# Optimization experiments

Hardware: AMD Instinct MI355X
Metric: run time of the kernel (lower is better)

Reference implementation:

```python
import jax, jax.numpy as jnp
import numpy as np

B = 4096   # batch
C = 1024   # per-node channels


def setup_inputs() -> dict:
    key = jax.random.key(0)
    k0, k1, k2, k3, k4 = jax.random.split(key, 5)
    x0 = jax.random.normal(k0, (B, C), dtype=jnp.float32)
    x1 = jax.random.normal(k1, (B, C), dtype=jnp.float32)
    # per-edge DNet weights: edge_in=concat (2 heads -> 2C) -> matmul W -> edge_out=split (2 tails of C)
    scale = 0.02
    W0 = jax.random.normal(k2, (2 * C, 2 * C), dtype=jnp.float32) * scale
    W1 = jax.random.normal(k3, (2 * C, 2 * C), dtype=jnp.float32) * scale
    W2 = jax.random.normal(k4, (2 * C, 2 * C), dtype=jnp.float32) * scale
    return {"x0": x0, "x1": x1, "W0": W0, "W1": W1, "W2": W2}


def _edge(head_a, head_b, W):
    # MHD_concat over sorted head nodes (dim=1), DNet matmul, MHD_split into tail node channels
    z = jnp.concatenate([head_a, head_b], axis=1) @ W  # [B, 2C]
    return z[:, :C], z[:, C:]  # two tail tensors [B, C]


def reference(x0, x1, W0, W1, W2):
    # DAG routing in topological order (MHD_topological_sort of the role matrix):
    # edge0: heads (n0, n1) -> tails (n2, n3)
    # edge1: heads (n2, n3) -> tails (n4, n5)
    # edge2: heads (n4, n5) -> tails (n6, n7)
    # node_tail_func = 'sum' (single contribution per tail here)
    n2, n3 = _edge(x0, x1, W0)
    n4, n5 = _edge(n2, n3, W1)
    n6, n7 = _edge(n4, n5, W2)
    # output: concat of terminal nodes (sorted order)
    return jnp.concatenate([n6, n7], axis=1)  # [B, 2C]
```

## Files before the change

kernel.cpp:

```cpp
#include <hip/hip_runtime.h>
#include <hip/hip_bf16.h>
#include <stdint.h>

typedef __bf16 bf16;
typedef __bf16 bf16x8 __attribute__((ext_vector_type(8)));
typedef float f32x4 __attribute__((ext_vector_type(4)));

#define GAS __attribute__((address_space(1)))
#define LAS __attribute__((address_space(3)))

static constexpr int M = 4096;
static constexpr int N = 2048;
static constexpr int K = 2048;

static constexpr int BM = 128, BN = 256, BK = 64;
static constexpr int NT = K / BK;
static constexpr int A_ELE = BM * BK;
static constexpr int B_ELE = BN * BK;
static constexpr int BUF_ELE = A_ELE + B_ELE;

static constexpr int WA_ELE = 64 * BK;
static constexpr int WB_ELE = 128 * BK;
static constexpr int WBUF_ELE = WA_ELE + WB_ELE;

__device__ __forceinline__ void gload_lds16(const bf16* gsrc, bf16* ldst) {
    __builtin_amdgcn_global_load_lds((const GAS void*)gsrc, (LAS void*)ldst, 16, 0, 0);
}

__global__ __launch_bounds__(256) void prep_kernel(const float* __restrict__ x0,
                                                   const float* __restrict__ x1,
                                                   const float* __restrict__ W0,
                                                   const float* __restrict__ W1,
                                                   const float* __restrict__ W2,
                                                   bf16* __restrict__ Xpk,
                                                   bf16* __restrict__ W0pk,
                                                   bf16* __restrict__ W1t,
                                                   bf16* __restrict__ W2t) {
    __shared__ bf16 tile[32][33];
    int bid = blockIdx.x;
    int tid = threadIdx.x;
    if (bid < 4096) {
        int idx = (bid * 256 + tid) * 8;
        int b = idx >> 11;
        int c = idx & 2047;
        const float* src = (c < 1024) ? (x0 + (size_t)b * 1024 + c)
                                      : (x1 + (size_t)b * 1024 + (c - 1024));
        float4 v0 = *reinterpret_cast<const float4*>(src);
        float4 v1 = *reinterpret_cast<const float4*>(src + 4);
        bf16x8 o;
        o[0] = (bf16)v0.x; o[1] = (bf16)v0.y; o[2] = (bf16)v0.z; o[3] = (bf16)v0.w;
        o[4] = (bf16)v1.x; o[5] = (bf16)v1.y; o[6] = (bf16)v1.z; o[7] = (bf16)v1.w;
        *reinterpret_cast<bf16x8*>(Xpk + idx) = o;
    } else if (bid < 6144) {
        int idx = ((bid - 4096) * 256 + tid) * 8;
        float4 v0 = *reinterpret_cast<const float4*>(W0 + idx);
        float4 v1 = *reinterpret_cast<const float4*>(W0 + idx + 4);
        bf16x8 o;
        o[0] = (bf16)v0.x; o[1] = (bf16)v0.y; o[2] = (bf16)v0.z; o[3] = (bf16)v0.w;
        o[4] = (bf16)v1.x; o[5] = (bf16)v1.y; o[6] = (bf16)v1.z; o[7] = (bf16)v1.w;
        *reinterpret_cast<bf16x8*>(W0pk + idx) = o;
    } else {
        int r = bid - 6144;
        int w = r >> 12;
        int t = r & 4095;
        const float* W  = (w == 0) ? W1  : W2;
        bf16*        Wt = (w == 0) ? W1t : W2t;
        int n0 = (t & 63) * 32;
        int k0 = (t >> 6) * 32;
        int tx = tid & 31;
        int ty = tid >> 5;
        #pragma unroll
        for (int i = 0; i < 4; i++) {
            int k = ty + i * 8;
            tile[k][tx] = (bf16)W[(size_t)(k0 + k) * N + n0 + tx];
        }
        __syncthreads();
        #pragma unroll
        for (int i = 0; i < 4; i++) {
            int n = ty + i * 8;
            Wt[(size_t)(n0 + n) * K + k0 + tx] = tile[tx][n];
        }
    }
}

__device__ __forceinline__ void read_frags(const bf16* __restrict__ ba, const bf16* __restrict__ bb,
                                           int aoff, int boff, int slot,
                                           bf16x8 af[4], bf16x8 bv[4]) {
    #pragma unroll
    for (int mi = 0; mi < 4; mi++)
        af[mi] = *reinterpret_cast<const bf16x8*>(ba + aoff + mi * 1024 + slot);
    #pragma unroll
    for (int ni = 0; ni < 4; ni++)
        bv[ni] = *reinterpret_cast<const bf16x8*>(bb + boff + ni * 1024 + slot);
}

__device__ __forceinline__ void do_mfma16(const bf16x8 af[4], const bf16x8 bv[4], f32x4 acc[4][4]) {
    __builtin_amdgcn_s_setprio(1);
    #pragma unroll
    for (int mi = 0; mi < 4; mi++)
        #pragma unroll
        for (int ni = 0; ni < 4; ni++)
            acc[mi][ni] = __builtin_amdgcn_mfma_f32_16x16x32_bf16(af[mi], bv[ni], acc[mi][ni], 0, 0, 0);
    __builtin_amdgcn_s_setprio(0);
}

__global__ __launch_bounds__(512, 2) void gemmx_kernel(const bf16* __restrict__ A,
                                                       const bf16* __restrict__ Bt,
                                                       float* __restrict__ Cout) {
    __shared__ bf16 lds[3 * BUF_ELE];

    int bid = blockIdx.x;
    int cpx = gridDim.x >> 3;
    int swz = (bid & 7) * cpx + (bid >> 3);
    int tm = swz >> 3;
    int tn = swz & 7;

    int tid  = threadIdx.x;
    int wave = tid >> 6;
    int lane = tid & 63;
    int wr = wave >> 2;
    int wc = wave & 3;
    int fr = lane & 15;
    int fb = lane >> 4;

    int srow = wave * 8 + (lane >> 3);
    int scol = ((lane & 7) ^ (lane >> 3)) * 8;
    const bf16* aS = A  + (size_t)(tm * BM + srow) * K + scol;
    const bf16* bS = Bt + (size_t)(tn * BN + srow) * K + scol;
    int sdst = wave * 512;

    int aoff  = (wr * 64 + fr) * 64;
    int boff  = (wc * 64 + fr) * 64;
    int slot0 = ((fb) ^ (fr & 7)) * 8;
    int slot1 = ((4 | fb) ^ (fr & 7)) * 8;

    f32x4 acc[4][4] = {};

    auto STAGE = [&](int bi, int t) {
        bf16* ba = (bf16*)lds + bi * BUF_ELE;
        bf16* bb = ba + A_ELE;
        const bf16* a = aS + t * BK;
        const bf16* b = bS + t * BK;
        gload_lds16(a,           ba + sdst);
        gload_lds16(a + 64 * K,  ba + sdst + 4096);
        gload_lds16(b,           bb + sdst);
        gload_lds16(b + 64 * K,  bb + sdst + 4096);
        gload_lds16(b + 128 * K, bb + sdst + 8192);
        gload_lds16(b + 192 * K, bb + sdst + 12288);
    };

    STAGE(0, 0);
    STAGE(1, 1);
    asm volatile("s_waitcnt vmcnt(6)" ::: "memory");
    __builtin_amdgcn_s_barrier();

    bf16x8 af0[4], bv0[4], af1[4], bv1[4];
    int cur = 0;
    for (int t = 0; t < NT - 2; ++t) {
        const bf16* ba = (const bf16*)lds + cur * BUF_ELE;
        const bf16* bb = ba + A_ELE;
        int sb = cur + 2; if (sb >= 3) sb -= 3;

        read_frags(ba, bb, aoff, boff, slot0, af0, bv0);
        read_frags(ba, bb, aoff, boff, slot1, af1, bv1);
        STAGE(sb, t + 2);
        asm volatile("s_waitcnt lgkmcnt(8)" ::: "memory");
        __builtin_amdgcn_sched_barrier(0);
        do_mfma16(af0, bv0, acc);
        asm volatile("s_waitcnt lgkmcnt(0)" ::: "memory");
        __builtin_amdgcn_sched_barrier(0);
        do_mfma16(af1, bv1, acc);
        asm volatile("s_waitcnt vmcnt(6)" ::: "memory");
        __builtin_amdgcn_s_barrier();
        cur = cur + 1; if (cur >= 3) cur -= 3;
    }
    {
        const bf16* ba = (const bf16*)lds + cur * BUF_ELE;
        const bf16* bb = ba + A_ELE;
        read_frags(ba, bb, aoff, boff, slot0, af0, bv0);
        read_frags(ba, bb, aoff, boff, slot1, af1, bv1);
        asm volatile("s_waitcnt lgkmcnt(8)" ::: "memory");
        __builtin_amdgcn_sched_barrier(0);
        do_mfma16(af0, bv0, acc);
        asm volatile("s_waitcnt lgkmcnt(0)" ::: "memory");
        __builtin_amdgcn_sched_barrier(0);
        do_mfma16(af1, bv1, acc);
        asm volatile("s_waitcnt vmcnt(0)" ::: "memory");
        __builtin_amdgcn_s_barrier();
        cur = cur + 1; if (cur >= 3) cur -= 3;
    }
    {
        const bf16* ba = (const bf16*)lds + cur * BUF_ELE;
        const bf16* bb = ba + A_ELE;
        read_frags(ba, bb, aoff, boff, slot0, af0, bv0);
        read_frags(ba, bb, aoff, boff, slot1, af1, bv1);
        asm volatile("s_waitcnt lgkmcnt(8)" ::: "memory");
        __builtin_amdgcn_sched_barrier(0);
        do_mfma16(af0, bv0, acc);
        asm volatile("s_waitcnt lgkmcnt(0)" ::: "memory");
        __builtin_amdgcn_sched_barrier(0);
        do_mfma16(af1, bv1, acc);
    }

    int row0 = tm * BM + wr * 64 + (lane >> 4) * 4;
    int col0 = tn * BN + wc * 64 + (lane & 15);
    #pragma unroll
    for (int mi = 0; mi < 4; mi++)
        #pragma unroll
        for (int r = 0; r < 4; r++) {
            size_t base = (size_t)(row0 + mi * 16 + r) * N + col0;
            #pragma unroll
            for (int ni = 0; ni < 4; ni++)
                Cout[base + ni * 16] = acc[mi][ni][r];
        }
}

__global__ __launch_bounds__(256, 2) void gemmw_kernel(const bf16* __restrict__ A,
                                                       const bf16* __restrict__ Bt,
                                                       bf16* __restrict__ C) {
    __shared__ bf16 lds[3 * WBUF_ELE];

    int bid = blockIdx.x;
    int cpx = gridDim.x >> 3;
    int swz = (bid & 7) * cpx + (bid >> 3);
    int tm = swz >> 4;
    int tn = swz & 15;

    int tid  = threadIdx.x;
    int wave = tid >> 6;
    int lane = tid & 63;
    int wr = wave >> 1;
    int wc = wave & 1;
    int fr = lane & 15;
    int fb = lane >> 4;

    int srow = tid >> 3;
    int scol = ((tid & 7) ^ (srow & 7)) * 8;
    const bf16* aS = A  + (size_t)(tm * 64  + srow) * K + scol;
    const bf16* bS = Bt + (size_t)(tn * 128 + srow) * K + scol;
    int sdst = wave * 512;

    int aoff  = (wr * 32 + fr) * 64;
    int boff  = (wc * 64 + fr) * 64;
    int slot0 = ((fb) ^ (fr & 7)) * 8;
    int slot1 = ((4 | fb) ^ (fr & 7)) * 8;

    f32x4 acc[2][4] = {};

    auto STAGE = [&](int bi, int t) {
        bf16* ba = (bf16*)lds + bi * WBUF_ELE;
        bf16* bb = ba + WA_ELE;
        const bf16* a = aS + t * BK;
        const bf16* b = bS + t * BK;
        gload_lds16(a,          ba + sdst);
        gload_lds16(a + 32 * K, ba + sdst + 2048);
        #pragma unroll
        for (int c = 0; c < 4; c++)
            gload_lds16(b + (size_t)c * 32 * K, bb + sdst + c * 2048);
    };

    auto READ = [&](const bf16* ba, const bf16* bb, int slot, bf16x8 af[2], bf16x8 bv[4]) {
        af[0] = *reinterpret_cast<const bf16x8*>(ba + aoff + slot);
        af[1] = *reinterpret_cast<const bf16x8*>(ba + aoff + 1024 + slot);
        #pragma unroll
        for (int ni = 0; ni < 4; ni++)
            bv[ni] = *reinterpret_cast<const bf16x8*>(bb + boff + ni * 1024 + slot);
    };

    auto MFMA8 = [&](const bf16x8 af[2], const bf16x8 bv[4]) {
        __builtin_amdgcn_s_setprio(1);
        #pragma unroll
        for (int mi = 0; mi < 2; mi++)
            #pragma unroll
            for (int ni = 0; ni < 4; ni++)
                acc[mi][ni] = __builtin_amdgcn_mfma_f32_16x16x32_bf16(af[mi], bv[ni], acc[mi][ni], 0, 0, 0);
        __builtin_amdgcn_s_setprio(0);
    };

    STAGE(0, 0);
    STAGE(1, 1);
    asm volatile("s_waitcnt vmcnt(6)" ::: "memory");
    __builtin_amdgcn_s_barrier();

    bf16x8 af0[2], bv0[4], af1[2], bv1[4];
    int cur = 0;
    for (int t = 0; t < NT - 2; ++t) {
        const bf16* ba = (const bf16*)lds + cur * WBUF_ELE;
        const bf16* bb = ba + WA_ELE;
        int sb = cur + 2; if (sb >= 3) sb -= 3;

        READ(ba, bb, slot0, af0, bv0);
        READ(ba, bb, slot1, af1, bv1);
        STAGE(sb, t + 2);
        asm volatile("s_waitcnt lgkmcnt(6)" ::: "memory");
        __builtin_amdgcn_sched_barrier(0);
        MFMA8(af0, bv0);
        asm volatile("s_waitcnt lgkmcnt(0)" ::: "memory");
        __builtin_amdgcn_sched_barrier(0);
        MFMA8(af1, bv1);
        asm volatile("s_waitcnt vmcnt(6)" ::: "memory");
        __builtin_amdgcn_s_barrier();
        cur = cur + 1; if (cur >= 3) cur -= 3;
    }
    {
        const bf16* ba = (const bf16*)lds + cur * WBUF_ELE;
        const bf16* bb = ba + WA_ELE;
        READ(ba, bb, slot0, af0, bv0);
        READ(ba, bb, slot1, af1, bv1);
        asm volatile("s_waitcnt lgkmcnt(6)" ::: "memory");
        __builtin_amdgcn_sched_barrier(0);
        MFMA8(af0, bv0);
        asm volatile("s_waitcnt lgkmcnt(0)" ::: "memory");
        __builtin_amdgcn_sched_barrier(0);
        MFMA8(af1, bv1);
        asm volatile("s_waitcnt vmcnt(0)" ::: "memory");
        __builtin_amdgcn_s_barrier();
        cur = cur + 1; if (cur >= 3) cur -= 3;
    }
    {
        const bf16* ba = (const bf16*)lds + cur * WBUF_ELE;
        const bf16* bb = ba + WA_ELE;
        READ(ba, bb, slot0, af0, bv0);
        READ(ba, bb, slot1, af1, bv1);
        asm volatile("s_waitcnt lgkmcnt(6)" ::: "memory");
        __builtin_amdgcn_sched_barrier(0);
        MFMA8(af0, bv0);
        asm volatile("s_waitcnt lgkmcnt(0)" ::: "memory");
        __builtin_amdgcn_sched_barrier(0);
        MFMA8(af1, bv1);
    }

    int row0 = tm * 64 + wr * 32 + (lane >> 4) * 4;
    int col0 = tn * 128 + wc * 64 + fr;
    #pragma unroll
    for (int mi = 0; mi < 2; mi++)
        #pragma unroll
        for (int r = 0; r < 4; r++) {
            size_t base = (size_t)(row0 + mi * 16 + r) * 2048 + col0;
            #pragma unroll
            for (int ni = 0; ni < 4; ni++)
                C[base + ni * 16] = (bf16)acc[mi][ni][r];
        }
}

extern "C" void kernel_launch(void* const* d_in, const int* in_sizes, int n_in,
                              void* d_out, int out_size, void* d_ws, size_t ws_size,
                              hipStream_t stream) {
    const float* x0 = (const float*)d_in[0];
    const float* x1 = (const float*)d_in[1];
    const float* W0 = (const float*)d_in[2];
    const float* W1 = (const float*)d_in[3];
    const float* W2 = (const float*)d_in[4];

    char* ws = (char*)d_ws;
    const size_t MB = 1024 * 1024;
    bf16* Xpk    = (bf16*)(ws + 0 * MB);
    bf16* W1t    = (bf16*)(ws + 16 * MB);
    bf16* W012t  = (bf16*)(ws + 16 * MB);
    bf16* W2t    = (bf16*)(ws + 24 * MB);
    bf16* W01    = (bf16*)(ws + 32 * MB);
    bf16* W0pk   = (bf16*)d_out;

    prep_kernel<<<4096 + 2048 + 2 * 4096, 256, 0, stream>>>(x0, x1, W0, W1, W2,
                                                            Xpk, W0pk, W1t, W2t);

    gemmw_kernel<<<(2048 / 64) * (2048 / 128), 256, 0, stream>>>(W0pk, W1t, W01);
    gemmw_kernel<<<(2048 / 64) * (2048 / 128), 256, 0, stream>>>(W2t, W01, W012t);
    gemmx_kernel<<<(M / BM) * (N / BN), 512, 0, stream>>>(Xpk, W012t, (float*)d_out);
}
```

Measured before the change: 101.1 us.

## Fold W2 transpose and x packing into the weight GEMM launches

Splits the monolithic prep kernel so that W2's transpose runs as extra blocks inside the first weight-product GEMM launch, and the x0/x1 bf16 packing runs as extra blocks inside the second. Weight-GEMM blocks can then overlap with independent memory-bound conversion work, filling idle CUs in the 512-block GEMM grids. The GEMM main loops are also manually unrolled by three with constant buffer indices, and the split lgkmcnt waits and sched barriers between the two MFMA halves are dropped. This leaves instruction ordering to the compiler and may change how LDS reads overlap with MFMAs.

After: 101.2 us. About the same (+0.0%).

```diff
diff --git a/kernel.cpp b/kernel.cpp
--- a/kernel.cpp
+++ b/kernel.cpp
@@ -22,86 +22,194 @@
 static constexpr int WA_ELE = 64 * BK;
 static constexpr int WB_ELE = 128 * BK;
 static constexpr int WBUF_ELE = WA_ELE + WB_ELE;
+static constexpr int WGRID = 512;
 
 __device__ __forceinline__ void gload_lds16(const bf16* gsrc, bf16* ldst) {
     __builtin_amdgcn_global_load_lds((const GAS void*)gsrc, (LAS void*)ldst, 16, 0, 0);
 }
 
-__global__ __launch_bounds__(256) void prep_kernel(const float* __restrict__ x0,
-                                                   const float* __restrict__ x1,
-                                                   const float* __restrict__ W0,
-                                                   const float* __restrict__ W1,
-                                                   const float* __restrict__ W2,
-                                                   bf16* __restrict__ Xpk,
-                                                   bf16* __restrict__ W0pk,
-                                                   bf16* __restrict__ W1t,
-                                                   bf16* __restrict__ W2t) {
+__device__ __forceinline__ void pack8(const float* __restrict__ src, bf16* __restrict__ dst) {
+    float4 v0 = *reinterpret_cast<const float4*>(src);
+    float4 v1 = *reinterpret_cast<const float4*>(src + 4);
+    bf16x8 o;
+    o[0] = (bf16)v0.x; o[1] = (bf16)v0.y; o[2] = (bf16)v0.z; o[3] = (bf16)v0.w;
+    o[4] = (bf16)v1.x; o[5] = (bf16)v1.y; o[6] = (bf16)v1.z; o[7] = (bf16)v1.w;
+    *reinterpret_cast<bf16x8*>(dst) = o;
+}
+
+__device__ __forceinline__ void transpose_tile(const float* __restrict__ W, bf16* __restrict__ Wt,
+                                               int t, int tid, bf16 (*tile)[33]) {
+    int n0 = (t & 63) * 32;
+    int k0 = (t >> 6) * 32;
+    int tx = tid & 31;
+    int ty = tid >> 5;
+    #pragma unroll
+    for (int i = 0; i < 4; i++) {
+        int k = ty + i * 8;
+        tile[k][tx] = (bf16)W[(size_t)(k0 + k) * N + n0 + tx];
+    }
+    __syncthreads();
+    #pragma unroll
+    for (int i = 0; i < 4; i++) {
+        int n = ty + i * 8;
+        Wt[(size_t)(n0 + n) * K + k0 + tx] = tile[tx][n];
+    }
+}
+
+__device__ __forceinline__ void gemmw_body(const bf16* __restrict__ A,
+                                           const bf16* __restrict__ Bt,
+                                           bf16* __restrict__ C,
+                                           int bid, bf16* lds) {
+    int swz = (bid & 7) * (WGRID >> 3) + (bid >> 3);
+    int tm = swz >> 4;
+    int tn = swz & 15;
+
+    int tid  = threadIdx.x;
+    int wave = tid >> 6;
+    int lane = tid & 63;
+    int wr = wave >> 1;
+    int wc = wave & 1;
+    int fr = lane & 15;
+    int fb = lane >> 4;
+
+    int srow = tid >> 3;
+    int scol = ((tid & 7) ^ (srow & 7)) * 8;
+    const bf16* aS = A  + (size_t)(tm * 64  + srow) * K + scol;
+    const bf16* bS = Bt + (size_t)(tn * 128 + srow) * K + scol;
+    int sdst = wave * 512;
+
+    int aoff  = (wr * 32 + fr) * 64;
+    int boff  = (wc * 64 + fr) * 64;
+    int slot0 = ((fb) ^ (fr & 7)) * 8;
+    int slot1 = ((4 | fb) ^ (fr & 7)) * 8;
+
+    f32x4 acc[2][4] = {};
+    bf16x8 af0[2], bv0[4], af1[2], bv1[4];
+
+    auto STAGE = [&](int bi, int t) {
+        bf16* ba = lds + bi * WBUF_ELE;
+        bf16* bb = ba + WA_ELE;
+        const bf16* a = aS + t * BK;
+        const bf16* b = bS + t * BK;
+        gload_lds16(a,          ba + sdst);
+        gload_lds16(a + 32 * K, ba + sdst + 2048);
+        #pragma unroll
+        for (int c = 0; c < 4; c++)
+            gload_lds16(b + (size_t)c * 32 * K, bb + sdst + c * 2048);
+    };
+    auto READ = [&](const bf16* ba, const bf16* bb, int slot, bf16x8 af[2], bf16x8 bv[4]) {
+        af[0] = *reinterpret_cast<const bf16x8*>(ba + aoff + slot);
+        af[1] = *reinterpret_cast<const bf16x8*>(ba + aoff + 1024 + slot);
+        #pragma unroll
+        for (int ni = 0; ni < 4; ni++)
+            bv[ni] = *reinterpret_cast<const bf16x8*>(bb + boff + ni * 1024 + slot);
+    };
+    auto MFMA8 = [&](const bf16x8 af[2], const bf16x8 bv[4]) {
+        #pragma unroll
+        for (int mi = 0; mi < 2; mi++)
+            #pragma unroll
+            for (int ni = 0; ni < 4; ni++)
+                acc[mi][ni] = __builtin_amdgcn_mfma_f32_16x16x32_bf16(af[mi], bv[ni], acc[mi][ni], 0, 0, 0);
+    };
+    auto TILE = [&](int t, int cb, int sb) {
+        const bf16* ba = lds + cb * WBUF_ELE;
+        const bf16* bb = ba + WA_ELE;
+        READ(ba, bb, slot0, af0, bv0);
+        READ(ba, bb, slot1, af1, bv1);
+        STAGE(sb, t + 2);
+        __builtin_amdgcn_s_setprio(1);
+        MFMA8(af0, bv0);
+        MFMA8(af1, bv1);
+        __builtin_amdgcn_s_setprio(0);
+        asm volatile("s_waitcnt lgkmcnt(0)" ::: "memory");
+        asm volatile("s_waitcnt vmcnt(6)" ::: "memory");
+        __builtin_amdgcn_s_barrier();
+    };
+
+    STAGE(0, 0);
+    STAGE(1, 1);
+    asm volatile("s_waitcnt vmcnt(6)" ::: "memory");
+    __builtin_amdgcn_s_barrier();
+
+    for (int i = 0; i < 10; ++i) {
+        TILE(3 * i,     0, 2);
+        TILE(3 * i + 1, 1, 0);
+        TILE(3 * i + 2, 2, 1);
+    }
+    {
+        const bf16* ba = lds;
+        const bf16* bb = ba + WA_ELE;
+        READ(ba, bb, slot0, af0, bv0);
+        READ(ba, bb, slot1, af1, bv1);
+        MFMA8(af0, bv0);
+        MFMA8(af1, bv1);
+        asm volatile("s_waitcnt lgkmcnt(0)" ::: "memory");
+        asm volatile("s_waitcnt vmcnt(0)" ::: "memory");
+        __builtin_amdgcn_s_barrier();
+    }
+    {
+        const bf16* ba = lds + WBUF_ELE;
+        const bf16* bb = ba + WA_ELE;
+        READ(ba, bb, slot0, af0, bv0);
+        READ(ba, bb, slot1, af1, bv1);
+        MFMA8(af0, bv0);
+        MFMA8(af1, bv1);
+    }
+
+    int row0 = tm * 64 + wr * 32 + (lane >> 4) * 4;
+    int col0 = tn * 128 + wc * 64 + fr;
+    #pragma unroll
+    for (int mi = 0; mi < 2; mi++)
+        #pragma unroll
+        for (int r = 0; r < 4; r++) {
+            size_t base = (size_t)(row0 + mi * 16 + r) * 2048 + col0;
+            #pragma unroll
+            for (int ni = 0; ni < 4; ni++)
+                C[base + ni * 16] = (bf16)acc[mi][ni][r];
+        }
+}
+
+__global__ __launch_bounds__(256) void k1_prep(const float* __restrict__ W0, bf16* __restrict__ W0pk,
+                                               const float* __restrict__ W1, bf16* __restrict__ W1t) {
     __shared__ bf16 tile[32][33];
     int bid = blockIdx.x;
     int tid = threadIdx.x;
-    if (bid < 4096) {
+    if (bid < 2048) {
         int idx = (bid * 256 + tid) * 8;
+        pack8(W0 + idx, W0pk + idx);
+    } else {
+        transpose_tile(W1, W1t, bid - 2048, tid, tile);
+    }
+}
+
+__global__ __launch_bounds__(256, 2) void g1_fused(const bf16* __restrict__ A, const bf16* __restrict__ Bt,
+                                                   bf16* __restrict__ C,
+                                                   const float* __restrict__ W2, bf16* __restrict__ W2t) {
+    __shared__ bf16 lds[3 * WBUF_ELE];
+    int bid = blockIdx.x;
+    if (bid < WGRID) {
+        gemmw_body(A, Bt, C, bid, lds);
+    } else {
+        transpose_tile(W2, W2t, bid - WGRID, threadIdx.x, (bf16(*)[33])lds);
+    }
+}
+
+__global__ __launch_bounds__(256, 2) void g2_fused(const bf16* __restrict__ A, const bf16* __restrict__ Bt,
+                                                   bf16* __restrict__ C,
+                                                   const float* __restrict__ x0, const float* __restrict__ x1,
+                                                   bf16* __restrict__ Xpk) {
+    __shared__ bf16 lds[3 * WBUF_ELE];
+    int bid = blockIdx.x;
+    if (bid < WGRID) {
+        gemmw_body(A, Bt, C, bid, lds);
+    } else {
+        int idx = ((bid - WGRID) * 256 + threadIdx.x) * 8;
         int b = idx >> 11;
         int c = idx & 2047;
         const float* src = (c < 1024) ? (x0 + (size_t)b * 1024 + c)
                                       : (x1 + (size_t)b * 1024 + (c - 1024));
-        float4 v0 = *reinterpret_cast<const float4*>(src);
-        float4 v1 = *reinterpret_cast<const float4*>(src + 4);
-        bf16x8 o;
-        o[0] = (bf16)v0.x; o[1] = (bf16)v0.y; o[2] = (bf16)v0.z; o[3] = (bf16)v0.w;
-        o[4] = (bf16)v1.x; o[5] = (bf16)v1.y; o[6] = (bf16)v1.z; o[7] = (bf16)v1.w;
-        *reinterpret_cast<bf16x8*>(Xpk + idx) = o;
-    } else if (bid < 6144) {
-        int idx = ((bid - 4096) * 256 + tid) * 8;
-        float4 v0 = *reinterpret_cast<const float4*>(W0 + idx);
-        float4 v1 = *reinterpret_cast<const float4*>(W0 + idx + 4);
-        bf16x8 o;
-        o[0] = (bf16)v0.x; o[1] = (bf16)v0.y; o[2] = (bf16)v0.z; o[3] = (bf16)v0.w;
-        o[4] = (bf16)v1.x; o[5] = (bf16)v1.y; o[6] = (bf16)v1.z; o[7] = (bf16)v1.w;
-        *reinterpret_cast<bf16x8*>(W0pk + idx) = o;
-    } else {
-        int r = bid - 6144;
-        int w = r >> 12;
-        int t = r & 4095;
-        const float* W  = (w == 0) ? W1  : W2;
-        bf16*        Wt = (w == 0) ? W1t : W2t;
-        int n0 = (t & 63) * 32;
-        int k0 = (t >> 6) * 32;
-        int tx = tid & 31;
-        int ty = tid >> 5;
-        #pragma unroll
-        for (int i = 0; i < 4; i++) {
-            int k = ty + i * 8;
-            tile[k][tx] = (bf16)W[(size_t)(k0 + k) * N + n0 + tx];
-        }
-        __syncthreads();
-        #pragma unroll
-        for (int i = 0; i < 4; i++) {
-            int n = ty + i * 8;
-            Wt[(size_t)(n0 + n) * K + k0 + tx] = tile[tx][n];
-        }
-    }
-}
-
-__device__ __forceinline__ void read_frags(const bf16* __restrict__ ba, const bf16* __restrict__ bb,
-                                           int aoff, int boff, int slot,
-                                           bf16x8 af[4], bf16x8 bv[4]) {
-    #pragma unroll
-    for (int mi = 0; mi < 4; mi++)
-        af[mi] = *reinterpret_cast<const bf16x8*>(ba + aoff + mi * 1024 + slot);
-    #pragma unroll
-    for (int ni = 0; ni < 4; ni++)
-        bv[ni] = *reinterpret_cast<const bf16x8*>(bb + boff + ni * 1024 + slot);
-}
-
-__device__ __forceinline__ void do_mfma16(const bf16x8 af[4], const bf16x8 bv[4], f32x4 acc[4][4]) {
-    __builtin_amdgcn_s_setprio(1);
-    #pragma unroll
-    for (int mi = 0; mi < 4; mi++)
-        #pragma unroll
-        for (int ni = 0; ni < 4; ni++)
-            acc[mi][ni] = __builtin_amdgcn_mfma_f32_16x16x32_bf16(af[mi], bv[ni], acc[mi][ni], 0, 0, 0);
-    __builtin_amdgcn_s_setprio(0);
+        pack8(src, Xpk + idx);
+    }
 }
 
 __global__ __launch_bounds__(512, 2) void gemmx_kernel(const bf16* __restrict__ A,
@@ -135,6 +243,7 @@
     int slot1 = ((4 | fb) ^ (fr & 7)) * 8;
 
     f32x4 acc[4][4] = {};
+    bf16x8 af0[4], bv0[4], af1[4], bv1[4];
 
     auto STAGE = [&](int bi, int t) {
         bf16* ba = (bf16*)lds + bi * BUF_ELE;
@@ -148,58 +257,64 @@
         gload_lds16(b + 128 * K, bb + sdst + 8192);
         gload_lds16(b + 192 * K, bb + sdst + 12288);
     };
+    auto READ = [&](const bf16* ba, const bf16* bb, int slot, bf16x8 af[4], bf16x8 bv[4]) {
+        #pragma unroll
+        for (int mi = 0; mi < 4; mi++)
+            af[mi] = *reinterpret_cast<const bf16x8*>(ba + aoff + mi * 1024 + slot);
+        #pragma unroll
+        for (int ni = 0; ni < 4; ni++)
+            bv[ni] = *reinterpret_cast<const bf16x8*>(bb + boff + ni * 1024 + slot);
+    };
+    auto MFMA16 = [&](const bf16x8 af[4], const bf16x8 bv[4]) {
+        #pragma unroll
+        for (int mi = 0; mi < 4; mi++)
+            #pragma unroll
+            for (int ni = 0; ni < 4; ni++)
+                acc[mi][ni] = __builtin_amdgcn_mfma_f32_16x16x32_bf16(af[mi], bv[ni], acc[mi][ni], 0, 0, 0);
+    };
+    auto TILE = [&](int t, int cb, int sb) {
+        const bf16* ba = (const bf16*)lds + cb * BUF_ELE;
+        const bf16* bb = ba + A_ELE;
+        READ(ba, bb, slot0, af0, bv0);
+        READ(ba, bb, slot1, af1, bv1);
+        STAGE(sb, t + 2);
+        __builtin_amdgcn_s_setprio(1);
+        MFMA16(af0, bv0);
+        MFMA16(af1, bv1);
+        __builtin_amdgcn_s_setprio(0);
+        asm volatile("s_waitcnt lgkmcnt(0)" ::: "memory");
+        asm volatile("s_waitcnt vmcnt(6)" ::: "memory");
+        __builtin_amdgcn_s_barrier();
+    };
 
     STAGE(0, 0);
     STAGE(1, 1);
     asm volatile("s_waitcnt vmcnt(6)" ::: "memory");
     __builtin_amdgcn_s_barrier();
 
-    bf16x8 af0[4], bv0[4], af1[4], bv1[4];
-    int cur = 0;
-    for (int t = 0; t < NT - 2; ++t) {
-        const bf16* ba = (const bf16*)lds + cur * BUF_ELE;
+    for (int i = 0; i < 10; ++i) {
+        TILE(3 * i,     0, 2);
+        TILE(3 * i + 1, 1, 0);
+        TILE(3 * i + 2, 2, 1);
+    }
+    {
+        const bf16* ba = (const bf16*)lds;
         const bf16* bb = ba + A_ELE;
-        int sb = cur + 2; if (sb >= 3) sb -= 3;
-
-        read_frags(ba, bb, aoff, boff, slot0, af0, bv0);
-        read_frags(ba, bb, aoff, boff, slot1, af1, bv1);
-        STAGE(sb, t + 2);
-        asm volatile("s_waitcnt lgkmcnt(8)" ::: "memory");
-        __builtin_amdgcn_sched_barrier(0);
-        do_mfma16(af0, bv0, acc);
+        READ(ba, bb, slot0, af0, bv0);
+        READ(ba, bb, slot1, af1, bv1);
+        MFMA16(af0, bv0);
+        MFMA16(af1, bv1);
         asm volatile("s_waitcnt lgkmcnt(0)" ::: "memory");
-        __builtin_amdgcn_sched_barrier(0);
-        do_mfma16(af1, bv1, acc);
-        asm volatile("s_waitcnt vmcnt(6)" ::: "memory");
-        __builtin_amdgcn_s_barrier();
-        cur = cur + 1; if (cur >= 3) cur -= 3;
-    }
-    {
-        const bf16* ba = (const bf16*)lds + cur * BUF_ELE;
-        const bf16* bb = ba + A_ELE;
-        read_frags(ba, bb, aoff, boff, slot0, af0, bv0);
-        read_frags(ba, bb, aoff, boff, slot1, af1, bv1);
-        asm volatile("s_waitcnt lgkmcnt(8)" ::: "memory");
-        __builtin_amdgcn_sched_barrier(0);
-        do_mfma16(af0, bv0, acc);
-        asm volatile("s_waitcnt lgkmcnt(0)" ::: "memory");
-        __builtin_amdgcn_sched_barrier(0);
-        do_mfma16(af1, bv1, acc);
         asm volatile("s_waitcnt vmcnt(0)" ::: "memory");
         __builtin_amdgcn_s_barrier();
-        cur = cur + 1; if (cur >= 3) cur -= 3;
     }
     {
-        const bf16* ba = (const bf16*)lds + cur * BUF_ELE;
+        const bf16* ba = (const bf16*)lds + BUF_ELE;
         const bf16* bb = ba + A_ELE;
-        read_frags(ba, bb, aoff, boff, slot0, af0, bv0);
-        read_frags(ba, bb, aoff, boff, slot1, af1, bv1);
-        asm volatile("s_waitcnt lgkmcnt(8)" ::: "memory");
-        __builtin_amdgcn_sched_barrier(0);
-        do_mfma16(af0, bv0, acc);
-        asm volatile("s_waitcnt lgkmcnt(0)" ::: "memory");
-        __builtin_amdgcn_sched_barrier(0);
-        do_mfma16(af1, bv1, acc);
+        READ(ba, bb, slot0, af0, bv0);
+        READ(ba, bb, slot1, af1, bv1);
+        MFMA16(af0, bv0);
+        MFMA16(af1, bv1);
     }
 
     int row0 = tm * BM + wr * 64 + (lane >> 4) * 4;
@@ -212,134 +327,6 @@
             #pragma unroll
             for (int ni = 0; ni < 4; ni++)
                 Cout[base + ni * 16] = acc[mi][ni][r];
-        }
-}
-
-__global__ __launch_bounds__(256, 2) void gemmw_kernel(const bf16* __restrict__ A,
-                                                       const bf16* __restrict__ Bt,
-                                                       bf16* __restrict__ C) {
-    __shared__ bf16 lds[3 * WBUF_ELE];
-
-    int bid = blockIdx.x;
-    int cpx = gridDim.x >> 3;
-    int swz = (bid & 7) * cpx + (bid >> 3);
-    int tm = swz >> 4;
-    int tn = swz & 15;
-
-    int tid  = threadIdx.x;
-    int wave = tid >> 6;
-    int lane = tid & 63;
-    int wr = wave >> 1;
-    int wc = wave & 1;
-    int fr = lane & 15;
-    int fb = lane >> 4;
-
-    int srow = tid >> 3;
-    int scol = ((tid & 7) ^ (srow & 7)) * 8;
-    const bf16* aS = A  + (size_t)(tm * 64  + srow) * K + scol;
-    const bf16* bS = Bt + (size_t)(tn * 128 + srow) * K + scol;
-    int sdst = wave * 512;
-
-    int aoff  = (wr * 32 + fr) * 64;
-    int boff  = (wc * 64 + fr) * 64;
-    int slot0 = ((fb) ^ (fr & 7)) * 8;
-    int slot1 = ((4 | fb) ^ (fr & 7)) * 8;
-
-    f32x4 acc[2][4] = {};
-
-    auto STAGE = [&](int bi, int t) {
-        bf16* ba = (bf16*)lds + bi * WBUF_ELE;
-        bf16* bb = ba + WA_ELE;
-        const bf16* a = aS + t * BK;
-        const bf16* b = bS + t * BK;
-        gload_lds16(a,          ba + sdst);
-        gload_lds16(a + 32 * K, ba + sdst + 2048);
-        #pragma unroll
-        for (int c = 0; c < 4; c++)
-            gload_lds16(b + (size_t)c * 32 * K, bb + sdst + c * 2048);
-    };
-
-    auto READ = [&](const bf16* ba, const bf16* bb, int slot, bf16x8 af[2], bf16x8 bv[4]) {
-        af[0] = *reinterpret_cast<const bf16x8*>(ba + aoff + slot);
-        af[1] = *reinterpret_cast<const bf16x8*>(ba + aoff + 1024 + slot);
-        #pragma unroll
-        for (int ni = 0; ni < 4; ni++)
-            bv[ni] = *reinterpret_cast<const bf16x8*>(bb + boff + ni * 1024 + slot);
-    };
-
-    auto MFMA8 = [&](const bf16x8 af[2], const bf16x8 bv[4]) {
-        __builtin_amdgcn_s_setprio(1);
-        #pragma unroll
-        for (int mi = 0; mi < 2; mi++)
-            #pragma unroll
-            for (int ni = 0; ni < 4; ni++)
-                acc[mi][ni] = __builtin_amdgcn_mfma_f32_16x16x32_bf16(af[mi], bv[ni], acc[mi][ni], 0, 0, 0);
-        __builtin_amdgcn_s_setprio(0);
-    };
-
-    STAGE(0, 0);
-    STAGE(1, 1);
-    asm volatile("s_waitcnt vmcnt(6)" ::: "memory");
-    __builtin_amdgcn_s_barrier();
-
-    bf16x8 af0[2], bv0[4], af1[2], bv1[4];
-    int cur = 0;
-    for (int t = 0; t < NT - 2; ++t) {
-        const bf16* ba = (const bf16*)lds + cur * WBUF_ELE;
-        const bf16* bb = ba + WA_ELE;
-        int sb = cur + 2; if (sb >= 3) sb -= 3;
-
-        READ(ba, bb, slot0, af0, bv0);
-        READ(ba, bb, slot1, af1, bv1);
-        STAGE(sb, t + 2);
-        asm volatile("s_waitcnt lgkmcnt(6)" ::: "memory");
-        __builtin_amdgcn_sched_barrier(0);
-        MFMA8(af0, bv0);
-        asm volatile("s_waitcnt lgkmcnt(0)" ::: "memory");
-        __builtin_amdgcn_sched_barrier(0);
-        MFMA8(af1, bv1);
-        asm volatile("s_waitcnt vmcnt(6)" ::: "memory");
-        __builtin_amdgcn_s_barrier();
-        cur = cur + 1; if (cur >= 3) cur -= 3;
-    }
-    {
-        const bf16* ba = (const bf16*)lds + cur * WBUF_ELE;
-        const bf16* bb = ba + WA_ELE;
-        READ(ba, bb, slot0, af0, bv0);
-        READ(ba, bb, slot1, af1, bv1);
-        asm volatile("s_waitcnt lgkmcnt(6)" ::: "memory");
-        __builtin_amdgcn_sched_barrier(0);
-        MFMA8(af0, bv0);
-        asm volatile("s_waitcnt lgkmcnt(0)" ::: "memory");
-        __builtin_amdgcn_sched_barrier(0);
-        MFMA8(af1, bv1);
-        asm volatile("s_waitcnt vmcnt(0)" ::: "memory");
-        __builtin_amdgcn_s_barrier();
-        cur = cur + 1; if (cur >= 3) cur -= 3;
-    }
-    {
-        const bf16* ba = (const bf16*)lds + cur * WBUF_ELE;
-        const bf16* bb = ba + WA_ELE;
-        READ(ba, bb, slot0, af0, bv0);
-        READ(ba, bb, slot1, af1, bv1);
-        asm volatile("s_waitcnt lgkmcnt(6)" ::: "memory");
-        __builtin_amdgcn_sched_barrier(0);
-        MFMA8(af0, bv0);
-        asm volatile("s_waitcnt lgkmcnt(0)" ::: "memory");
-        __builtin_amdgcn_sched_barrier(0);
-        MFMA8(af1, bv1);
-    }
-
-    int row0 = tm * 64 + wr * 32 + (lane >> 4) * 4;
-    int col0 = tn * 128 + wc * 64 + fr;
-    #pragma unroll
-    for (int mi = 0; mi < 2; mi++)
-        #pragma unroll
-        for (int r = 0; r < 4; r++) {
-            size_t base = (size_t)(row0 + mi * 16 + r) * 2048 + col0;
-            #pragma unroll
-            for (int ni = 0; ni < 4; ni++)
-                C[base + ni * 16] = (bf16)acc[mi][ni][r];
         }
 }
 
@@ -361,10 +348,8 @@
     bf16* W01    = (bf16*)(ws + 32 * MB);
     bf16* W0pk   = (bf16*)d_out;
 
-    prep_kernel<<<4096 + 2048 + 2 * 4096, 256, 0, stream>>>(x0, x1, W0, W1, W2,
-                                                            Xpk, W0pk, W1t, W2t);
-
-    gemmw_kernel<<<(2048 / 64) * (2048 / 128), 256, 0, stream>>>(W0pk, W1t, W01);
-    gemmw_kernel<<<(2048 / 64) * (2048 / 128), 256, 0, stream>>>(W2t, W01, W012t);
+    k1_prep<<<2048 + 4096, 256, 0, stream>>>(W0, W0pk, W1, W1t);
+    g1_fused<<<WGRID + 4096, 256, 0, stream>>>(W0pk, W1t, W01, W2, W2t);
+    g2_fused<<<WGRID + 4096, 256, 0, stream>>>(W2t, W01, W012t, x0, x1, Xpk);
     gemmx_kernel<<<(M / BM) * (N / BN), 512, 0, stream>>>(Xpk, W012t, (float*)d_out);
 }
```
